# Kernel tuning notes

Hardware: AMD Instinct MI355X
Metric: run time of the kernel (lower is better)

## Reference

```python
import jax, jax.numpy as jnp
import numpy as np
import math

HIDDEN = 2048
N_Q = 16
N_KV = 8
HEAD_DIM = 128
THETA = 10000.0
RANK = 8
ALPHA = 16
LORA_SCALING = ALPHA / RANK  # 2.0
SCALING = 1.0 / math.sqrt(HEAD_DIM)


def setup_inputs() -> dict:
    key = jax.random.key(0)
    ks = jax.random.split(key, 14)
    B, S = 2, 2048
    std = 0.02
    inp = {
        "x": jax.random.normal(ks[0], (B, S, HIDDEN), dtype=jnp.float32),
        # nn.Linear weights: [out_features, in_features]
        "Wq": jax.random.normal(ks[1], (N_Q * HEAD_DIM, HIDDEN), dtype=jnp.float32) * std,
        "Wk": jax.random.normal(ks[2], (N_KV * HEAD_DIM, HIDDEN), dtype=jnp.float32) * std,
        "Wv": jax.random.normal(ks[3], (N_KV * HEAD_DIM, HIDDEN), dtype=jnp.float32) * std,
        "Wo": jax.random.normal(ks[4], (HIDDEN, N_Q * HEAD_DIM), dtype=jnp.float32) * std,
        "qA": jax.random.normal(ks[5], (RANK, HIDDEN), dtype=jnp.float32) * std,
        "qB": jax.random.normal(ks[6], (N_Q * HEAD_DIM, RANK), dtype=jnp.float32) * std,
        "kA": jax.random.normal(ks[7], (RANK, HIDDEN), dtype=jnp.float32) * std,
        "kB": jax.random.normal(ks[8], (N_KV * HEAD_DIM, RANK), dtype=jnp.float32) * std,
        "vA": jax.random.normal(ks[9], (RANK, HIDDEN), dtype=jnp.float32) * std,
        "vB": jax.random.normal(ks[10], (N_KV * HEAD_DIM, RANK), dtype=jnp.float32) * std,
        "oA": jax.random.normal(ks[11], (RANK, N_Q * HEAD_DIM), dtype=jnp.float32) * std,
        "oB": jax.random.normal(ks[12], (HIDDEN, RANK), dtype=jnp.float32) * std,
    }
    return inp


def _rope_cos_sin(seq_len, dtype):
    inv_freq = 1.0 / (THETA ** (jnp.arange(0, HEAD_DIM, 2, dtype=jnp.float32) / HEAD_DIM))
    t = jnp.arange(seq_len, dtype=jnp.float32)
    freqs = t[:, None] * inv_freq[None, :]  # [S, D/2]
    return jnp.cos(freqs).astype(dtype), jnp.sin(freqs).astype(dtype)


def _apply_rope(x, cos, sin):
    # x: [B, H, S, D]; interleaved real/imag pairs on last dim
    xr = x[..., ::2]
    xi = x[..., 1::2]
    rr = xr * cos - xi * sin
    ri = xr * sin + xi * cos
    return jnp.stack([rr, ri], axis=-1).reshape(x.shape)


def _forward(x, Wq, Wk, Wv, Wo, qA, qB, kA, kB, vA, vB, oA, oB):
    B, S, H = x.shape
    # base projections + LoRA (low-rank path kept factored: (x @ A^T) @ B^T)
    q = x @ Wq.T + ((x @ qA.T) @ qB.T) * LORA_SCALING  # [B,S,NQ*D]
    k = x @ Wk.T + ((x @ kA.T) @ kB.T) * LORA_SCALING  # [B,S,NKV*D]
    v = x @ Wv.T + ((x @ vA.T) @ vB.T) * LORA_SCALING
    q = q.reshape(B, S, N_Q, HEAD_DIM).transpose(0, 2, 1, 3)   # [B,NQ,S,D]
    k = k.reshape(B, S, N_KV, HEAD_DIM).transpose(0, 2, 1, 3)  # [B,NKV,S,D]
    v = v.reshape(B, S, N_KV, HEAD_DIM).transpose(0, 2, 1, 3)
    cos, sin = _rope_cos_sin(S, x.dtype)  # [S, D/2] each
    q = _apply_rope(q, cos, sin)
    k = _apply_rope(k, cos, sin)
    if N_Q != N_KV:
        rep = N_Q // N_KV
        k = jnp.repeat(k, rep, axis=1)  # [B,NQ,S,D]
        v = jnp.repeat(v, rep, axis=1)
    scores = jnp.einsum('bhqd,bhkd->bhqk', q, k) * SCALING
    causal = jnp.tril(jnp.ones((S, S), dtype=bool))
    scores = jnp.where(causal, scores, -jnp.inf)
    attn = jax.nn.softmax(scores, axis=-1).astype(v.dtype)
    out = jnp.einsum('bhqk,bhkd->bhqd', attn, v)  # [B,NQ,S,D]
    out = out.transpose(0, 2, 1, 3).reshape(B, S, N_Q * HEAD_DIM)
    return out @ Wo.T + ((out @ oA.T) @ oB.T) * LORA_SCALING


def reference(x, Wq, Wk, Wv, Wo, qA, qB, kA, kB, vA, vB, oA, oB):
    return _forward(x, Wq, Wk, Wv, Wo, qA, qB, kA, kB, vA, vB, oA, oB)
```

## Files before the change

### kernel.cpp

```cpp
#include <hip/hip_runtime.h>
#include <hip/hip_bf16.h>
#include <cmath>

#define HIDDEN 2048
#define SEQ 2048
#define BATCH 2
#define NQ 16
#define NKV 8
#define HD 128
#define RANKL 8
#define LORA_SCALE 2.0f
#define INV_SQRT_D 0.08838834764831845f
#define LOG2E 1.4426950408889634f
#define SM_SCALE (INV_SQRT_D * LOG2E)

typedef unsigned short ushort_t;
typedef __bf16 bf16x8 __attribute__((ext_vector_type(8)));
typedef float f32x4 __attribute__((ext_vector_type(4)));

static __device__ __forceinline__ ushort_t f2bf(float f) {
    __hip_bfloat16 h = __float2bfloat16(f);
    return *(ushort_t*)&h;
}
static __device__ __forceinline__ float bf2f(ushort_t u) {
    unsigned int v = ((unsigned int)u) << 16;
    return __builtin_bit_cast(float, v);
}
static __device__ __forceinline__ void gload_lds16(const ushort_t* g, ushort_t* l) {
    __builtin_amdgcn_global_load_lds(
        (const __attribute__((address_space(1))) unsigned int*)g,
        (__attribute__((address_space(3))) unsigned int*)l, 16, 0, 0);
}

__global__ __launch_bounds__(256) void lora_cast_x(
    const float* __restrict__ X, ushort_t* __restrict__ Xbf,
    const float* __restrict__ qA, const float* __restrict__ kA,
    const float* __restrict__ vA,
    float* __restrict__ oq, float* __restrict__ ok, float* __restrict__ ov)
{
    int m = blockIdx.x;
    int t = threadIdx.x;
    int c0 = t * 8;
    const float* xr = X + (size_t)m * HIDDEN + c0;
    float4 a = *(const float4*)xr;
    float4 b = *(const float4*)(xr + 4);
    float xv[8] = {a.x, a.y, a.z, a.w, b.x, b.y, b.z, b.w};
    uint4 o;
    o.x = (unsigned int)f2bf(xv[0]) | ((unsigned int)f2bf(xv[1]) << 16);
    o.y = (unsigned int)f2bf(xv[2]) | ((unsigned int)f2bf(xv[3]) << 16);
    o.z = (unsigned int)f2bf(xv[4]) | ((unsigned int)f2bf(xv[5]) << 16);
    o.w = (unsigned int)f2bf(xv[6]) | ((unsigned int)f2bf(xv[7]) << 16);
    *(uint4*)(Xbf + (size_t)m * HIDDEN + c0) = o;

    float p[3][RANKL];
#pragma unroll
    for (int w = 0; w < 3; w++)
#pragma unroll
        for (int r = 0; r < RANKL; r++) p[w][r] = 0.f;
    const float* Aw[3] = {qA, kA, vA};
#pragma unroll
    for (int e = 0; e < 8; e++) {
        float x8 = xv[e];
#pragma unroll
        for (int w = 0; w < 3; w++)
#pragma unroll
            for (int r = 0; r < RANKL; r++)
                p[w][r] += x8 * Aw[w][r * HIDDEN + c0 + e];
    }
#pragma unroll
    for (int w = 0; w < 3; w++)
#pragma unroll
        for (int r = 0; r < RANKL; r++) {
            float v = p[w][r];
            v += __shfl_xor(v, 32); v += __shfl_xor(v, 16);
            v += __shfl_xor(v, 8);  v += __shfl_xor(v, 4);
            v += __shfl_xor(v, 2);  v += __shfl_xor(v, 1);
            p[w][r] = v;
        }
    __shared__ float wred[4][3][RANKL];
    int wave = t >> 6, lane = t & 63;
    if (lane == 0) {
#pragma unroll
        for (int w = 0; w < 3; w++)
#pragma unroll
            for (int r = 0; r < RANKL; r++) wred[wave][w][r] = p[w][r];
    }
    __syncthreads();
    if (t < 3 * RANKL) {
        int w = t / RANKL, r = t % RANKL;
        float s = wred[0][w][r] + wred[1][w][r] + wred[2][w][r] + wred[3][w][r];
        float* dst = (w == 0) ? oq : (w == 1) ? ok : ov;
        dst[(size_t)m * RANKL + r] = s;
    }
}

__global__ __launch_bounds__(256) void lora_xa_bf16(
    const ushort_t* __restrict__ X, const float* __restrict__ Aw,
    float* __restrict__ out, int K)
{
    int m = blockIdx.x;
    int t = threadIdx.x;
    const ushort_t* xr = X + (size_t)m * K;
    float p[RANKL];
#pragma unroll
    for (int r = 0; r < RANKL; r++) p[r] = 0.f;
    for (int c = t; c < K; c += 256) {
        float xv = bf2f(xr[c]);
#pragma unroll
        for (int r = 0; r < RANKL; r++) p[r] += xv * Aw[r * K + c];
    }
#pragma unroll
    for (int r = 0; r < RANKL; r++) {
        float v = p[r];
        v += __shfl_xor(v, 32); v += __shfl_xor(v, 16);
        v += __shfl_xor(v, 8);  v += __shfl_xor(v, 4);
        v += __shfl_xor(v, 2);  v += __shfl_xor(v, 1);
        p[r] = v;
    }
    __shared__ float wred[4][RANKL];
    int wave = t >> 6, lane = t & 63;
    if (lane == 0) {
#pragma unroll
        for (int r = 0; r < RANKL; r++) wred[wave][r] = p[r];
    }
    __syncthreads();
    if (t < RANKL) {
        out[(size_t)m * RANKL + t] =
            wred[0][t] + wred[1][t] + wred[2][t] + wred[3][t];
    }
}

__global__ __launch_bounds__(256) void cast_weights(
    const float* __restrict__ Wq, const float* __restrict__ Wk,
    const float* __restrict__ Wv, const float* __restrict__ Wo,
    ushort_t* __restrict__ Wqb, ushort_t* __restrict__ Wkb,
    ushort_t* __restrict__ Wvb, ushort_t* __restrict__ Wob)
{
    size_t i = (size_t)blockIdx.x * 256 + threadIdx.x;
    const float* src; ushort_t* dst; size_t j;
    if (i < 524288)       { src = Wq; dst = Wqb; j = i; }
    else if (i < 786432)  { src = Wk; dst = Wkb; j = i - 524288; }
    else if (i < 1048576) { src = Wv; dst = Wvb; j = i - 786432; }
    else                  { src = Wo; dst = Wob; j = i - 1048576; }
    const float4* p = (const float4*)src + j * 2;
    float4 a = p[0], b = p[1];
    uint4 o;
    o.x = (unsigned int)f2bf(a.x) | ((unsigned int)f2bf(a.y) << 16);
    o.y = (unsigned int)f2bf(a.z) | ((unsigned int)f2bf(a.w) << 16);
    o.z = (unsigned int)f2bf(b.x) | ((unsigned int)f2bf(b.y) << 16);
    o.w = (unsigned int)f2bf(b.z) | ((unsigned int)f2bf(b.w) << 16);
    *(uint4*)(dst + j * 8) = o;
}

static __device__ __forceinline__ void gemm_core(
    const ushort_t* __restrict__ A, const ushort_t* __restrict__ B,
    void* __restrict__ Cout, int N, int K, int bm, int bn,
    const float* __restrict__ xa, const float* __restrict__ LB,
    float lscale, int out_bf16, ushort_t* As, ushort_t* Bs)
{
    const int t = threadIdx.x;
    const int lane = t & 63;
    const int w = t >> 6;
    const int quad = lane >> 4;
    const int c = lane & 15;

    const int wm = (w & 1) * 64;
    const int wn = (w >> 1) * 64;

    f32x4 acc[4][4];
#pragma unroll
    for (int i = 0; i < 4; i++)
#pragma unroll
        for (int j = 0; j < 4; j++) acc[i][j] = (f32x4){0.f, 0.f, 0.f, 0.f};

    const int p0 = w * 64 + lane;
    const int p1 = 256 + w * 64 + lane;
    const int r0 = p0 >> 2, g0 = (p0 & 3) ^ ((p0 >> 3) & 3);
    const int r1 = p1 >> 2, g1 = (p1 & 3) ^ ((p1 >> 3) & 3);
    const ushort_t* gA0 = A + (size_t)(bm + r0) * K + g0 * 8;
    const ushort_t* gA1 = A + (size_t)(bm + r1) * K + g1 * 8;
    const ushort_t* gB0 = B + (size_t)(bn + r0) * K + g0 * 8;
    const ushort_t* gB1 = B + (size_t)(bn + r1) * K + g1 * 8;
    ushort_t* lA0 = As + (size_t)(w * 64) * 8;
    ushort_t* lA1 = As + (size_t)(256 + w * 64) * 8;
    ushort_t* lB0 = Bs + (size_t)(w * 64) * 8;
    ushort_t* lB1 = Bs + (size_t)(256 + w * 64) * 8;

    const int csw = quad ^ ((c >> 1) & 3);

    for (int k0 = 0; k0 < K; k0 += 32) {
        __syncthreads();
        gload_lds16(gA0 + k0, lA0);
        gload_lds16(gA1 + k0, lA1);
        gload_lds16(gB0 + k0, lB0);
        gload_lds16(gB1 + k0, lB1);
        __syncthreads();

        bf16x8 af[4], bfr[4];
#pragma unroll
        for (int mt = 0; mt < 4; mt++)
            af[mt] = *(const bf16x8*)&As[((wm + mt * 16 + c) * 4 + csw) * 8];
#pragma unroll
        for (int nt = 0; nt < 4; nt++)
            bfr[nt] = *(const bf16x8*)&Bs[((wn + nt * 16 + c) * 4 + csw) * 8];
#pragma unroll
        for (int mt = 0; mt < 4; mt++)
#pragma unroll
            for (int nt = 0; nt < 4; nt++)
                acc[mt][nt] = __builtin_amdgcn_mfma_f32_16x16x32_bf16(
                    af[mt], bfr[nt], acc[mt][nt], 0, 0, 0);
    }

    float lb[4][RANKL];
#pragma unroll
    for (int nt = 0; nt < 4; nt++) {
        int col = bn + wn + nt * 16 + c;
        float4 u = *(const float4*)&LB[(size_t)col * RANKL];
        float4 v = *(const float4*)&LB[(size_t)col * RANKL + 4];
        lb[nt][0] = u.x; lb[nt][1] = u.y; lb[nt][2] = u.z; lb[nt][3] = u.w;
        lb[nt][4] = v.x; lb[nt][5] = v.y; lb[nt][6] = v.z; lb[nt][7] = v.w;
    }
#pragma unroll
    for (int mt = 0; mt < 4; mt++) {
        float la[4][RANKL];
#pragma unroll
        for (int r = 0; r < 4; r++) {
            int row = bm + wm + mt * 16 + quad * 4 + r;
            float4 u = *(const float4*)&xa[(size_t)row * RANKL];
            float4 v = *(const float4*)&xa[(size_t)row * RANKL + 4];
            la[r][0] = u.x; la[r][1] = u.y; la[r][2] = u.z; la[r][3] = u.w;
            la[r][4] = v.x; la[r][5] = v.y; la[r][6] = v.z; la[r][7] = v.w;
        }
#pragma unroll
        for (int nt = 0; nt < 4; nt++) {
#pragma unroll
            for (int r = 0; r < 4; r++) {
                float s = 0.f;
#pragma unroll
                for (int k = 0; k < RANKL; k++) s += la[r][k] * lb[nt][k];
                float val = acc[mt][nt][r] + lscale * s;
                size_t row = bm + wm + mt * 16 + quad * 4 + r;
                size_t col = bn + wn + nt * 16 + c;
                if (out_bf16)
                    ((ushort_t*)Cout)[row * N + col] = f2bf(val);
                else
                    ((float*)Cout)[row * N + col] = val;
            }
        }
    }
}

#define BKT 64
#define NKT (HIDDEN / BKT)

__global__ __launch_bounds__(512, 2) void gemm_qkv256(
    const ushort_t* __restrict__ A,
    const ushort_t* __restrict__ Wqb, const ushort_t* __restrict__ Wkb,
    const ushort_t* __restrict__ Wvb,
    ushort_t* __restrict__ q_lin, ushort_t* __restrict__ k_lin,
    ushort_t* __restrict__ v_lin,
    const float* __restrict__ xa_q, const float* __restrict__ xa_k,
    const float* __restrict__ xa_v,
    const float* __restrict__ qB, const float* __restrict__ kB,
    const float* __restrict__ vB)
{
    __shared__ __align__(16) ushort_t As[2][256 * BKT];
    __shared__ __align__(16) ushort_t Bs[2][256 * BKT];

    const int t = threadIdx.x;
    const int lane = t & 63;
    const int w = t >> 6;
    const int wm = w >> 2;
    const int wn = w & 3;
    const int quad = lane >> 4;
    const int c = lane & 15;
    const int c7 = c & 7;

    const int bc = blockIdx.y;
    const ushort_t* Bmat; ushort_t* Cout; const float* xa; const float* LB;
    int N, bn;
    if (bc < 8)       { Bmat = Wqb; Cout = q_lin; xa = xa_q; LB = qB; N = 2048; bn = bc * 256; }
    else if (bc < 12) { Bmat = Wkb; Cout = k_lin; xa = xa_k; LB = kB; N = 1024; bn = (bc - 8) * 256; }
    else              { Bmat = Wvb; Cout = v_lin; xa = xa_v; LB = vB; N = 1024; bn = (bc - 12) * 256; }
    const int bm = blockIdx.x * 256;

    const int r8  = lane >> 3;
    const int ksl = (lane & 7) ^ r8;
    const int ga  = wn;
    const int bh  = wn >> 1;
    const int gb  = wm * 2 + (wn & 1);

    const ushort_t* gAb = A    + (size_t)(bm + wm * 128 + ga * 8 + r8) * HIDDEN + ksl * 8;
    const ushort_t* gBb = Bmat + (size_t)(bn + bh * 128 + gb * 8 + r8) * HIDDEN + ksl * 8;
    const int lAoff = (wm * 128 + ga * 8) * BKT;
    const int lBoff = (bh * 128 + gb * 8) * BKT;

#pragma unroll
    for (int j = 0; j < 4; j++) {
        gload_lds16(gAb + (size_t)j * 32 * HIDDEN, &As[0][lAoff + j * 32 * BKT]);
        gload_lds16(gBb + (size_t)j * 32 * HIDDEN, &Bs[0][lBoff + j * 32 * BKT]);
    }
#pragma unroll
    for (int j = 0; j < 3; j++) {
        gload_lds16(gAb + (size_t)j * 32 * HIDDEN + BKT, &As[1][lAoff + j * 32 * BKT]);
        gload_lds16(gBb + (size_t)j * 32 * HIDDEN + BKT, &Bs[1][lBoff + j * 32 * BKT]);
    }

    f32x4 acc[8][4];
#pragma unroll
    for (int i = 0; i < 8; i++)
#pragma unroll
        for (int j = 0; j < 4; j++) acc[i][j] = (f32x4){0.f, 0.f, 0.f, 0.f};

#pragma unroll 1
    for (int T = 0; T < NKT; ++T) {
        const int cur = T & 1;
        const ushort_t* cA = As[cur];
        const ushort_t* cB = Bs[cur];
        bf16x8 bfr[4][2];

#pragma unroll
        for (int q = 0; q < 4; ++q) {
            if (q == 0) {
                asm volatile("s_waitcnt vmcnt(6)" ::: "memory");
            }
            __builtin_amdgcn_sched_barrier(0);
            __builtin_amdgcn_s_barrier();
            __builtin_amdgcn_sched_barrier(0);

            bf16x8 af[2][2];
#pragma unroll
            for (int m2 = 0; m2 < 2; ++m2) {
                const int row = wm * 128 + (q * 2 + m2) * 16 + c;
#pragma unroll
                for (int kh = 0; kh < 2; ++kh)
                    af[m2][kh] = *(const bf16x8*)
                        &cA[row * BKT + (((kh * 4 + quad) ^ c7) * 8)];
            }
            if (q == 0) {
#pragma unroll
                for (int nt = 0; nt < 4; ++nt) {
                    const int rowb = wn * 64 + nt * 16 + c;
#pragma unroll
                    for (int kh = 0; kh < 2; ++kh)
                        bfr[nt][kh] = *(const bf16x8*)
                            &cB[rowb * BKT + (((kh * 4 + quad) ^ c7) * 8)];
                }
            }

            if (q == 0) {
                const int tl = T + 1;
                if (tl < NKT) {
                    gload_lds16(gAb + (size_t)3 * 32 * HIDDEN + (size_t)tl * BKT,
                                &As[cur ^ 1][lAoff + 3 * 32 * BKT]);
                    gload_lds16(gBb + (size_t)3 * 32 * HIDDEN + (size_t)tl * BKT,
                                &Bs[cur ^ 1][lBoff + 3 * 32 * BKT]);
                }
            } else {
                const int tl = T + 2;
                if (tl < NKT) {
                    const int j = q - 1;
                    gload_lds16(gAb + (size_t)j * 32 * HIDDEN + (size_t)tl * BKT,
                                &As[cur][lAoff + j * 32 * BKT]);
                    gload_lds16(gBb + (size_t)j * 32 * HIDDEN + (size_t)tl * BKT,
                                &Bs[cur][lBoff + j * 32 * BKT]);
                }
            }

            __builtin_amdgcn_s_setprio(1);
#pragma unroll
            for (int m2 = 0; m2 < 2; ++m2)
#pragma unroll
                for (int nt = 0; nt < 4; ++nt)
#pragma unroll
                    for (int kh = 0; kh < 2; ++kh)
                        acc[q * 2 + m2][nt] = __builtin_amdgcn_mfma_f32_16x16x32_bf16(
                            af[m2][kh], bfr[nt][kh], acc[q * 2 + m2][nt], 0, 0, 0);
            __builtin_amdgcn_s_setprio(0);
        }
    }

    float lb[4][RANKL];
#pragma unroll
    for (int nt = 0; nt < 4; nt++) {
        int col = bn + wn * 64 + nt * 16 + c;
        float4 u = *(const float4*)&LB[(size_t)col * RANKL];
        float4 v = *(const float4*)&LB[(size_t)col * RANKL + 4];
        lb[nt][0] = u.x; lb[nt][1] = u.y; lb[nt][2] = u.z; lb[nt][3] = u.w;
        lb[nt][4] = v.x; lb[nt][5] = v.y; lb[nt][6] = v.z; lb[nt][7] = v.w;
    }
#pragma unroll
    for (int mt = 0; mt < 8; mt++) {
        float la[4][RANKL];
#pragma unroll
        for (int r = 0; r < 4; r++) {
            int row = bm + wm * 128 + mt * 16 + quad * 4 + r;
            float4 u = *(const float4*)&xa[(size_t)row * RANKL];
            float4 v = *(const float4*)&xa[(size_t)row * RANKL + 4];
            la[r][0] = u.x; la[r][1] = u.y; la[r][2] = u.z; la[r][3] = u.w;
            la[r][4] = v.x; la[r][5] = v.y; la[r][6] = v.z; la[r][7] = v.w;
        }
#pragma unroll
        for (int nt = 0; nt < 4; nt++) {
#pragma unroll
            for (int r = 0; r < 4; r++) {
                float s = 0.f;
#pragma unroll
                for (int k = 0; k < RANKL; k++) s += la[r][k] * lb[nt][k];
                float val = acc[mt][nt][r] + LORA_SCALE * s;
                size_t row = bm + wm * 128 + mt * 16 + quad * 4 + r;
                size_t col = bn + wn * 64 + nt * 16 + c;
                Cout[row * N + col] = f2bf(val);
            }
        }
    }
}

__global__ __launch_bounds__(256) void gemm_wo(
    const ushort_t* __restrict__ A, const ushort_t* __restrict__ Wob,
    float* __restrict__ out, const float* __restrict__ xa_o,
    const float* __restrict__ oB)
{
    __shared__ ushort_t As[128 * 32];
    __shared__ ushort_t Bs[128 * 32];
    gemm_core(A, Wob, out, HIDDEN, NQ * HD, blockIdx.x * 128, blockIdx.y * 128,
              xa_o, oB, LORA_SCALE, 0, As, Bs);
}

__global__ __launch_bounds__(256) void rope_qk(
    const ushort_t* __restrict__ qlin, const ushort_t* __restrict__ klin,
    ushort_t* __restrict__ qb, ushort_t* __restrict__ kb)
{
    int bs = blockIdx.x;
    int s = bs & (SEQ - 1);
    int b = bs >> 11;
    int t = threadIdx.x;
    int p = t & 63;
    float inv = exp2f(-(float)p * 0.20762050593046f);
    float ang = (float)s * inv;
    float cc = cosf(ang), si = sinf(ang);
#pragma unroll
    for (int j = 0; j < 6; j++) {
        int item = t + 256 * j;
        int hh = item >> 6;
        unsigned int pk;
        ushort_t* dst;
        if (hh < NQ) {
            pk = *(const unsigned int*)&qlin[(size_t)bs * (NQ * HD) + hh * HD + 2 * p];
            dst = qb + (((size_t)(b * NQ + hh) * SEQ) + s) * HD + 2 * p;
        } else {
            int kh = hh - NQ;
            pk = *(const unsigned int*)&klin[(size_t)bs * (NKV * HD) + kh * HD + 2 * p];
            dst = kb + (((size_t)(b * NKV + kh) * SEQ) + s) * HD + 2 * p;
        }
        float xr = bf2f((ushort_t)(pk & 0xffff));
        float xi = bf2f((ushort_t)(pk >> 16));
        float rr = xr * cc - xi * si;
        float ri = xr * si + xi * cc;
        *(unsigned int*)dst = ((unsigned int)f2bf(ri) << 16) | f2bf(rr);
    }
}

__global__ __launch_bounds__(256) void v_transpose(
    const ushort_t* __restrict__ vlin, ushort_t* __restrict__ Vt)
{
    int bk = blockIdx.x;
    int b = bk >> 3, kvh = bk & 7;
    int s0 = blockIdx.y * 64, d0 = blockIdx.z * 64;
    __shared__ ushort_t tile[64 * 72];
    int t = threadIdx.x;
#pragma unroll
    for (int i = 0; i < 2; i++) {
        int id = t + 256 * i;
        int r = id >> 3, cc = id & 7;
        uint4 v = *(const uint4*)&vlin[(size_t)(b * SEQ + s0 + r) * (NKV * HD)
                                       + kvh * HD + d0 + cc * 8];
        *(uint4*)&tile[r * 72 + cc * 8] = v;
    }
    __syncthreads();
#pragma unroll
    for (int i = 0; i < 2; i++) {
        int id = t + 256 * i;
        int dr = id >> 3, sc = id & 7;
        ushort_t tmp[8];
#pragma unroll
        for (int e = 0; e < 8; e++) tmp[e] = tile[(sc * 8 + e) * 72 + dr];
        *(uint4*)&Vt[((size_t)(b * NKV + kvh) * HD + d0 + dr) * SEQ + s0 + sc * 8]
            = *(uint4*)tmp;
    }
}

__global__ __launch_bounds__(256, 2) void attn_mfma3(
    const ushort_t* __restrict__ Q, const ushort_t* __restrict__ K,
    const ushort_t* __restrict__ V, ushort_t* __restrict__ O)
{
    __shared__ ushort_t Ks[2][64 * 128];
    __shared__ ushort_t Vs[2][128 * 64];
    __shared__ ushort_t Psh[4][16 * 68];

    const int t = threadIdx.x;
    const int lane = t & 63;
    const int w = t >> 6;
    const int quad = lane >> 4;
    const int c = lane & 15;
    const int q4 = quad * 4;
    const int c7 = c & 7;

    const int head = blockIdx.x >> 4;
    const int a = blockIdx.x & 15;
    const int h = head & (NQ - 1);
    const int b = head >> 4;
    const int kvh = b * NKV + (h >> 1);

    const ushort_t* Kg = K + (size_t)kvh * SEQ * HD;
    const ushort_t* Vg = V + (size_t)kvh * HD * SEQ;

    const ushort_t* gK[4]; const ushort_t* gV[4];
    int lo[4];
#pragma unroll
    for (int i = 0; i < 4; i++) {
        int cid = t + 256 * i;
        int kr = cid >> 4, kc = cid & 15;
        gK[i] = Kg + (size_t)kr * HD + ((kc ^ (kr & 7)) * 8);
        int vd = cid >> 3, vc = cid & 7;
        gV[i] = Vg + (size_t)vd * SEQ + ((vc ^ (vd & 7)) * 8);
        lo[i] = (i * 256 + (t & ~63)) * 8;
    }

#pragma unroll 1
    for (int half = 0; half < 2; half++) {
        const int qt = half ? (31 - a) : a;
        const int qb0 = qt * 64;
        const int myrow = qb0 + w * 16;

        const ushort_t* Qg = Q + ((size_t)head * SEQ + myrow + c) * HD;
        bf16x8 qf[4];
#pragma unroll
        for (int ch = 0; ch < 4; ch++)
            qf[ch] = *(const bf16x8*)(Qg + ch * 32 + quad * 8);

        f32x4 o[8];
#pragma unroll
        for (int i = 0; i < 8; i++) o[i] = (f32x4){0.f, 0.f, 0.f, 0.f};
        float lp[4] = {0.f, 0.f, 0.f, 0.f};

        const int ntiles = qt + 1;

#pragma unroll
        for (int i = 0; i < 4; i++) gload_lds16(gK[i], &Ks[0][lo[i]]);
#pragma unroll
        for (int i = 0; i < 4; i++) gload_lds16(gV[i], &Vs[0][lo[i]]);
        __syncthreads();

        for (int tile = 0; tile < ntiles; ++tile) {
            const int cur = tile & 1;
            if (tile + 1 < ntiles) {
                const int j1 = (tile + 1) * 64;
#pragma unroll
                for (int i = 0; i < 4; i++)
                    gload_lds16(gK[i] + (size_t)j1 * HD, &Ks[cur ^ 1][lo[i]]);
#pragma unroll
                for (int i = 0; i < 4; i++)
                    gload_lds16(gV[i] + j1, &Vs[cur ^ 1][lo[i]]);
            }

            f32x4 s[4];
#pragma unroll
            for (int tt = 0; tt < 4; tt++) s[tt] = (f32x4){0.f, 0.f, 0.f, 0.f};
#pragma unroll
            for (int tt = 0; tt < 4; tt++) {
                const int krow = tt * 16 + c;
#pragma unroll
                for (int ch = 0; ch < 4; ch++) {
                    bf16x8 kf = *(const bf16x8*)
                        &Ks[cur][krow * 128 + (((ch * 4 + quad) ^ c7) * 8)];
                    s[tt] = __builtin_amdgcn_mfma_f32_16x16x32_bf16(
                        qf[ch], kf, s[tt], 0, 0, 0);
                }
            }

            const bool diag = (tile == qt);
            const int j0 = tile * 64;
#pragma unroll
            for (int r = 0; r < 4; r++) {
                const int row_g = myrow + q4 + r;
#pragma unroll
                for (int tt = 0; tt < 4; tt++) {
                    float p = exp2f(s[tt][r] * SM_SCALE);
                    if (diag && (j0 + tt * 16 + c > row_g)) p = 0.f;
                    Psh[w][(q4 + r) * 68 + tt * 16 + c] = f2bf(p);
                    lp[r] += p;
                }
            }

            bf16x8 pf[2];
#pragma unroll
            for (int ch = 0; ch < 2; ch++) {
                int base = c * 68 + ch * 32 + quad * 8;
                uint2 aa = *(const uint2*)&Psh[w][base];
                uint2 bb = *(const uint2*)&Psh[w][base + 4];
                uint4 u; u.x = aa.x; u.y = aa.y; u.z = bb.x; u.w = bb.y;
                pf[ch] = __builtin_bit_cast(bf16x8, u);
            }

#pragma unroll
            for (int dt = 0; dt < 8; dt++) {
                const int vrow = dt * 16 + c;
#pragma unroll
                for (int ch = 0; ch < 2; ch++) {
                    bf16x8 vf = *(const bf16x8*)
                        &Vs[cur][vrow * 64 + (((ch * 4 + quad) ^ c7) * 8)];
                    o[dt] = __builtin_amdgcn_mfma_f32_16x16x32_bf16(
                        pf[ch], vf, o[dt], 0, 0, 0);
                }
            }
            __syncthreads();
        }

        float inv[4];
#pragma unroll
        for (int r = 0; r < 4; r++) {
            float v = lp[r];
            v += __shfl_xor(v, 1);
            v += __shfl_xor(v, 2);
            v += __shfl_xor(v, 4);
            v += __shfl_xor(v, 8);
            inv[r] = 1.f / v;
        }
        size_t base = ((size_t)b * SEQ + myrow + q4) * (NQ * HD) + h * HD + c;
#pragma unroll
        for (int r = 0; r < 4; r++)
#pragma unroll
            for (int dt = 0; dt < 8; dt++)
                O[base + (size_t)r * (NQ * HD) + dt * 16] =
                    f2bf(o[dt][r] * inv[r]);
    }
}

extern "C" void kernel_launch(void* const* d_in, const int* in_sizes, int n_in,
                              void* d_out, int out_size, void* d_ws, size_t ws_size,
                              hipStream_t stream)
{
    const float* x  = (const float*)d_in[0];
    const float* Wq = (const float*)d_in[1];
    const float* Wk = (const float*)d_in[2];
    const float* Wv = (const float*)d_in[3];
    const float* Wo = (const float*)d_in[4];
    const float* qA = (const float*)d_in[5];
    const float* qB = (const float*)d_in[6];
    const float* kA = (const float*)d_in[7];
    const float* kB = (const float*)d_in[8];
    const float* vA = (const float*)d_in[9];
    const float* vB = (const float*)d_in[10];
    const float* oA = (const float*)d_in[11];
    const float* oB = (const float*)d_in[12];
    float* out = (float*)d_out;
    float* ws = (float*)d_ws;

    const int M = BATCH * SEQ;

    float* xa_q = ws;
    float* xa_k = ws + 32768;
    float* xa_v = ws + 65536;
    float* xa_o = ws + 98304;
    ushort_t* q_lin = (ushort_t*)(ws + 131072);
    ushort_t* k_lin = (ushort_t*)(ws + 4325376);
    ushort_t* v_lin = (ushort_t*)(ws + 6422528);
    ushort_t* qb    = (ushort_t*)(ws + 8519680);
    ushort_t* kb    = (ushort_t*)(ws + 12713984);
    ushort_t* vtb   = (ushort_t*)(ws + 14811136);
    ushort_t* xbf   = (ushort_t*)(ws + 16908288);
    ushort_t* Wqb   = (ushort_t*)(ws + 21102592);
    ushort_t* Wkb   = (ushort_t*)(ws + 23199744);
    ushort_t* Wvb   = (ushort_t*)(ws + 24248320);
    ushort_t* Wob   = (ushort_t*)(ws + 25296896);
    ushort_t* attn_out = q_lin;

    lora_cast_x<<<M, 256, 0, stream>>>(x, xbf, qA, kA, vA, xa_q, xa_k, xa_v);

    cast_weights<<<6144, 256, 0, stream>>>(Wq, Wk, Wv, Wo, Wqb, Wkb, Wvb, Wob);

    gemm_qkv256<<<dim3(M / 256, 16), 512, 0, stream>>>(
        xbf, Wqb, Wkb, Wvb, q_lin, k_lin, v_lin,
        xa_q, xa_k, xa_v, qB, kB, vB);

    rope_qk<<<M, 256, 0, stream>>>(q_lin, k_lin, qb, kb);
    v_transpose<<<dim3(BATCH * NKV, SEQ / 64, HD / 64), 256, 0, stream>>>(v_lin, vtb);

    attn_mfma3<<<512, 256, 0, stream>>>(qb, kb, vtb, attn_out);

    lora_xa_bf16<<<M, 256, 0, stream>>>(attn_out, oA, xa_o, NQ * HD);
    gemm_wo<<<dim3(M / 128, HIDDEN / 128), 256, 0, stream>>>(
        attn_out, Wob, out, xa_o, oB);
}
```

Measured before the change: 393.2 us.

## Double attention query tile to 128 rows so each wave handles two subblocks

The attention kernel now processes 128 query rows per block instead of 64, with each wave computing two 16-row subblocks against every shared K/V tile. The aim is to halve the K/V global-to-LDS traffic and sync count per query row, and to raise MFMA work per LDS K/V fragment read. The cost is half as many blocks (256), which lowers occupancy and leaves less work for load balancing. It also roughly doubles the accumulator and Q-fragment registers per thread, which risks spills under the existing launch bounds.

```diff
diff --git a/kernel.cpp b/kernel.cpp
--- a/kernel.cpp
+++ b/kernel.cpp
@@ -490,7 +490,7 @@
     }
 }
 
-__global__ __launch_bounds__(256, 2) void attn_mfma3(
+__global__ __launch_bounds__(256, 2) void attn_mfma4(
     const ushort_t* __restrict__ Q, const ushort_t* __restrict__ K,
     const ushort_t* __restrict__ V, ushort_t* __restrict__ O)
 {
@@ -506,8 +506,8 @@
     const int q4 = quad * 4;
     const int c7 = c & 7;
 
-    const int head = blockIdx.x >> 4;
-    const int a = blockIdx.x & 15;
+    const int head = blockIdx.x >> 3;
+    const int a = blockIdx.x & 7;
     const int h = head & (NQ - 1);
     const int b = head >> 4;
     const int kvh = b * NKV + (h >> 1);
@@ -529,22 +529,27 @@
 
 #pragma unroll 1
     for (int half = 0; half < 2; half++) {
-        const int qt = half ? (31 - a) : a;
-        const int qb0 = qt * 64;
-        const int myrow = qb0 + w * 16;
-
-        const ushort_t* Qg = Q + ((size_t)head * SEQ + myrow + c) * HD;
-        bf16x8 qf[4];
-#pragma unroll
-        for (int ch = 0; ch < 4; ch++)
-            qf[ch] = *(const bf16x8*)(Qg + ch * 32 + quad * 8);
-
-        f32x4 o[8];
-#pragma unroll
-        for (int i = 0; i < 8; i++) o[i] = (f32x4){0.f, 0.f, 0.f, 0.f};
-        float lp[4] = {0.f, 0.f, 0.f, 0.f};
-
-        const int ntiles = qt + 1;
+        const int qt = half ? (15 - a) : a;
+        const int Q0 = qt * 128;
+        const int R0w = Q0 + w * 32;
+
+        bf16x8 qf[2][4];
+#pragma unroll
+        for (int qb = 0; qb < 2; qb++) {
+            const ushort_t* Qg = Q + ((size_t)head * SEQ + R0w + qb * 16 + c) * HD;
+#pragma unroll
+            for (int ch = 0; ch < 4; ch++)
+                qf[qb][ch] = *(const bf16x8*)(Qg + ch * 32 + quad * 8);
+        }
+
+        f32x4 o[2][8];
+#pragma unroll
+        for (int qb = 0; qb < 2; qb++)
+#pragma unroll
+            for (int i = 0; i < 8; i++) o[qb][i] = (f32x4){0.f, 0.f, 0.f, 0.f};
+        float lp[2][4] = {{0.f, 0.f, 0.f, 0.f}, {0.f, 0.f, 0.f, 0.f}};
+
+        const int ntiles = 2 * qt + 2;
 
 #pragma unroll
         for (int i = 0; i < 4; i++) gload_lds16(gK[i], &Ks[0][lo[i]]);
@@ -564,9 +569,12 @@
                     gload_lds16(gV[i] + j1, &Vs[cur ^ 1][lo[i]]);
             }
 
-            f32x4 s[4];
-#pragma unroll
-            for (int tt = 0; tt < 4; tt++) s[tt] = (f32x4){0.f, 0.f, 0.f, 0.f};
+            f32x4 s0[4], s1[4];
+#pragma unroll
+            for (int tt = 0; tt < 4; tt++) {
+                s0[tt] = (f32x4){0.f, 0.f, 0.f, 0.f};
+                s1[tt] = (f32x4){0.f, 0.f, 0.f, 0.f};
+            }
 #pragma unroll
             for (int tt = 0; tt < 4; tt++) {
                 const int krow = tt * 16 + c;
@@ -574,33 +582,39 @@
                 for (int ch = 0; ch < 4; ch++) {
                     bf16x8 kf = *(const bf16x8*)
                         &Ks[cur][krow * 128 + (((ch * 4 + quad) ^ c7) * 8)];
-                    s[tt] = __builtin_amdgcn_mfma_f32_16x16x32_bf16(
-                        qf[ch], kf, s[tt], 0, 0, 0);
+                    s0[tt] = __builtin_amdgcn_mfma_f32_16x16x32_bf16(
+                        qf[0][ch], kf, s0[tt], 0, 0, 0);
+                    s1[tt] = __builtin_amdgcn_mfma_f32_16x16x32_bf16(
+                        qf[1][ch], kf, s1[tt], 0, 0, 0);
                 }
             }
 
-            const bool diag = (tile == qt);
             const int j0 = tile * 64;
-#pragma unroll
-            for (int r = 0; r < 4; r++) {
-                const int row_g = myrow + q4 + r;
-#pragma unroll
-                for (int tt = 0; tt < 4; tt++) {
-                    float p = exp2f(s[tt][r] * SM_SCALE);
-                    if (diag && (j0 + tt * 16 + c > row_g)) p = 0.f;
-                    Psh[w][(q4 + r) * 68 + tt * 16 + c] = f2bf(p);
-                    lp[r] += p;
+            bf16x8 pf[2][2];
+#pragma unroll
+            for (int qb = 0; qb < 2; qb++) {
+                const int Rb = R0w + qb * 16;
+                const bool gate = (j0 + 63 > Rb);
+#pragma unroll
+                for (int r = 0; r < 4; r++) {
+                    const int row_g = Rb + q4 + r;
+#pragma unroll
+                    for (int tt = 0; tt < 4; tt++) {
+                        float sv = (qb == 0) ? s0[tt][r] : s1[tt][r];
+                        float p = exp2f(sv * SM_SCALE);
+                        if (gate && (j0 + tt * 16 + c > row_g)) p = 0.f;
+                        Psh[w][(q4 + r) * 68 + tt * 16 + c] = f2bf(p);
+                        lp[qb][r] += p;
+                    }
                 }
-            }
-
-            bf16x8 pf[2];
-#pragma unroll
-            for (int ch = 0; ch < 2; ch++) {
-                int base = c * 68 + ch * 32 + quad * 8;
-                uint2 aa = *(const uint2*)&Psh[w][base];
-                uint2 bb = *(const uint2*)&Psh[w][base + 4];
-                uint4 u; u.x = aa.x; u.y = aa.y; u.z = bb.x; u.w = bb.y;
-                pf[ch] = __builtin_bit_cast(bf16x8, u);
+#pragma unroll
+                for (int ch = 0; ch < 2; ch++) {
+                    int base = c * 68 + ch * 32 + quad * 8;
+                    uint2 aa = *(const uint2*)&Psh[w][base];
+                    uint2 bb = *(const uint2*)&Psh[w][base + 4];
+                    uint4 u; u.x = aa.x; u.y = aa.y; u.z = bb.x; u.w = bb.y;
+                    pf[qb][ch] = __builtin_bit_cast(bf16x8, u);
+                }
             }
 
 #pragma unroll
@@ -610,30 +624,36 @@
                 for (int ch = 0; ch < 2; ch++) {
                     bf16x8 vf = *(const bf16x8*)
                         &Vs[cur][vrow * 64 + (((ch * 4 + quad) ^ c7) * 8)];
-                    o[dt] = __builtin_amdgcn_mfma_f32_16x16x32_bf16(
-                        pf[ch], vf, o[dt], 0, 0, 0);
+                    o[0][dt] = __builtin_amdgcn_mfma_f32_16x16x32_bf16(
+                        pf[0][ch], vf, o[0][dt], 0, 0, 0);
+                    o[1][dt] = __builtin_amdgcn_mfma_f32_16x16x32_bf16(
+                        pf[1][ch], vf, o[1][dt], 0, 0, 0);
                 }
             }
             __syncthreads();
         }
 
-        float inv[4];
-#pragma unroll
-        for (int r = 0; r < 4; r++) {
-            float v = lp[r];
-            v += __shfl_xor(v, 1);
-            v += __shfl_xor(v, 2);
-            v += __shfl_xor(v, 4);
-            v += __shfl_xor(v, 8);
-            inv[r] = 1.f / v;
-        }
-        size_t base = ((size_t)b * SEQ + myrow + q4) * (NQ * HD) + h * HD + c;
-#pragma unroll
-        for (int r = 0; r < 4; r++)
-#pragma unroll
-            for (int dt = 0; dt < 8; dt++)
-                O[base + (size_t)r * (NQ * HD) + dt * 16] =
-                    f2bf(o[dt][r] * inv[r]);
+#pragma unroll
+        for (int qb = 0; qb < 2; qb++) {
+            float inv[4];
+#pragma unroll
+            for (int r = 0; r < 4; r++) {
+                float v = lp[qb][r];
+                v += __shfl_xor(v, 1);
+                v += __shfl_xor(v, 2);
+                v += __shfl_xor(v, 4);
+                v += __shfl_xor(v, 8);
+                inv[r] = 1.f / v;
+            }
+            size_t base = ((size_t)b * SEQ + R0w + qb * 16 + q4) * (NQ * HD)
+                          + h * HD + c;
+#pragma unroll
+            for (int r = 0; r < 4; r++)
+#pragma unroll
+                for (int dt = 0; dt < 8; dt++)
+                    O[base + (size_t)r * (NQ * HD) + dt * 16] =
+                        f2bf(o[qb][dt][r] * inv[r]);
+        }
     }
 }
 
@@ -687,7 +707,7 @@
     rope_qk<<<M, 256, 0, stream>>>(q_lin, k_lin, qb, kb);
     v_transpose<<<dim3(BATCH * NKV, SEQ / 64, HD / 64), 256, 0, stream>>>(v_lin, vtb);
 
-    attn_mfma3<<<512, 256, 0, stream>>>(qb, kb, vtb, attn_out);
+    attn_mfma4<<<256, 256, 0, stream>>>(qb, kb, vtb, attn_out);
 
     lora_xa_bf16<<<M, 256, 0, stream>>>(attn_out, oA, xa_o, NQ * HD);
     gemm_wo<<<dim3(M / 128, HIDDEN / 128), 256, 0, stream>>>(
```

Result: slower. 434.9 us (+10.6%).
